# Performance work log

Measured on AMD Instinct MI355X. Metric: run time of the kernel, lower is better.

## Reference

```python
import jax, jax.numpy as jnp
import numpy as np

IMG = 224
WS = 8      # windows_size
STRIDE = 2
M = 1

def _dct_mat(size):
    i = np.arange(size)[:, None]
    j = np.arange(size)[None, :]
    scale = np.where(i == 0, np.sqrt(1.0 / size), np.sqrt(2.0 / size))
    return (scale * np.cos((j + 0.5) * np.pi * i / size)).astype(np.float32)

def _gen_filter(start, end, size):
    i = np.arange(size)[:, None]
    j = np.arange(size)[None, :]
    s = i + j
    return np.where((s > end) | (s < start), 0.0, 1.0).astype(np.float32)

def setup_inputs() -> dict:
    key = jax.random.key(0)
    x = jax.random.normal(key, (16, 3, IMG, IMG), dtype=jnp.float32)
    D = jnp.asarray(_dct_mat(WS))                       # [ws, ws] DCT matrix
    filt = jnp.asarray(_gen_filter(WS // 3, WS * 2, WS))  # high-pass base filter
    return {"x": x, "D": D, "filt": filt}

def reference(x, D, filt):
    b, c, H, W = x.shape
    n = (H - WS) // STRIDE + 1                 # patches per side (109)
    rows = jnp.arange(n)[:, None] * STRIDE + jnp.arange(WS)[None, :]  # [n, ws]
    # unfold: overlapping stride-2 patches -> [b, n, n, c, ws, ws]
    p = x[:, :, rows, :]                       # [b, c, n, ws, W]
    p = p[..., rows]                           # [b, c, n, ws, n, ws]
    p = p.transpose(0, 2, 4, 1, 3, 5)          # [b, n, n, c, ws, ws]
    # block DCT: D @ p @ D^T
    xd = jnp.einsum('pi,bmncij,qj->bmncpq', D, p, D)
    # filter (use_learnable=False, norm=False -> plain elementwise mask)
    y = xd * filt
    # block IDCT: D^T @ y @ D
    y = jnp.einsum('pi,bmncpq,qj->bmncij', D, y, D)
    # fold: overlap-add scatter back to [b, c, H, W]
    hh = rows[:, None, :, None]                # [n,1,ws,1]
    ww = rows[None, :, None, :]                # [1,n,1,ws]
    flat = hh * W + ww                         # [n,n,ws,ws] flat spatial index
    y_t = y.transpose(0, 3, 1, 2, 4, 5)        # [b, c, n, n, ws, ws]
    out = jnp.zeros((b, c, H * W), x.dtype).at[:, :, flat].add(y_t)
    return out.reshape(b, c, H, W)             # m=1 -> cat is identity
```

## Files before the change

kernel.cpp:

```cpp
#include <hip/hip_runtime.h>

#define IMG 224
#define NP 109
#define BC 48
#define NPIX (IMG * IMG)
#define TILE 56
#define QT 28
#define PT 31
#define XR 68
#define XC2 34


#define LOAD_D_SCALARS(D)                                                  \
    const float d0_0 = (D)[0], d0_1 = (D)[1], d0_2 = (D)[2], d0_3 = (D)[3],\
                d0_4 = (D)[4], d0_5 = (D)[5], d0_6 = (D)[6], d0_7 = (D)[7];\
    const float d1_0 = (D)[8],  d1_1 = (D)[9],  d1_2 = (D)[10],            \
                d1_3 = (D)[11], d1_4 = (D)[12], d1_5 = (D)[13],            \
                d1_6 = (D)[14], d1_7 = (D)[15];

__global__ __launch_bounds__(256) void fused_dct_kernel(
    const float* __restrict__ x, const float* __restrict__ D,
    const float* __restrict__ filt, float* __restrict__ out)
{
    __shared__ float x_s[XR * XR];
    __shared__ float ca_s[PT * PT];
    __shared__ float cb_s[PT * PT];
    __shared__ float cc_s[PT * PT];

    const int tid = threadIdx.x;
    const int h0 = blockIdx.y * TILE;
    const int w0 = blockIdx.x * TILE;
    const int bc = blockIdx.z;

    LOAD_D_SCALARS(D)
    const float w00 = 1.0f - filt[0];
    const float w01 = 1.0f - filt[1];
    const float w10 = 1.0f - filt[8];

    const float* xb = x + (size_t)bc * NPIX;

    for (int i = tid; i < XR * XC2; i += 256) {
        int r  = i / XC2;
        int c2 = i - r * XC2;
        int gr = h0 - 6 + r;
        int gc = w0 - 6 + 2 * c2;
        float2 v = make_float2(0.f, 0.f);
        if ((unsigned)gr < (unsigned)IMG && (unsigned)gc < (unsigned)IMG)
            v = *(const float2*)(xb + (size_t)gr * IMG + gc);
        *(float2*)&x_s[r * XR + 2 * c2] = v;
    }
    __syncthreads();

    const int pr0 = (h0 >> 1) - 3;
    const int pc0 = (w0 >> 1) - 3;
    for (int p = tid; p < PT * PT; p += 256) {
        int prl = p / PT;
        int pcl = p - prl * PT;
        const float* wnd = &x_s[(2 * prl) * XR + 2 * pcl];
        float c00 = 0.f, c01 = 0.f, c10 = 0.f;

#define C_ROW(i)                                                               \
        {                                                                      \
            const float2* prow = (const float2*)(wnd + (i) * XR);              \
            float2 v0 = prow[0], v1 = prow[1], v2 = prow[2], v3 = prow[3];     \
            float s = fmaf(v0.x, d0_0, fmaf(v0.y, d0_1,                        \
                      fmaf(v1.x, d0_2, fmaf(v1.y, d0_3,                        \
                      fmaf(v2.x, d0_4, fmaf(v2.y, d0_5,                        \
                      fmaf(v3.x, d0_6, v3.y * d0_7)))))));                     \
            float t = fmaf(v0.x, d1_0, fmaf(v0.y, d1_1,                        \
                      fmaf(v1.x, d1_2, fmaf(v1.y, d1_3,                        \
                      fmaf(v2.x, d1_4, fmaf(v2.y, d1_5,                        \
                      fmaf(v3.x, d1_6, v3.y * d1_7)))))));                     \
            c00 = fmaf(d0_##i, s, c00);                                        \
            c01 = fmaf(d0_##i, t, c01);                                        \
            c10 = fmaf(d1_##i, s, c10);                                        \
        }

        C_ROW(0) C_ROW(1) C_ROW(2) C_ROW(3)
        C_ROW(4) C_ROW(5) C_ROW(6) C_ROW(7)
#undef C_ROW

        bool valid = ((unsigned)(pr0 + prl) < (unsigned)NP) &&
                     ((unsigned)(pc0 + pcl) < (unsigned)NP);
        float m = valid ? 1.0f : 0.0f;
        ca_s[p] = c00 * w00 * m;
        cb_s[p] = c01 * w01 * m;
        cc_s[p] = c10 * w10 * m;
    }
    __syncthreads();

    const int qh0 = h0 >> 1, qw0 = w0 >> 1;
    float* ob = out + (size_t)bc * NPIX;
    for (int q = tid; q < QT * QT; q += 256) {
        int qhl = q / QT;
        int qwl = q - qhl * QT;

        float aee = 0.f, aeo = 0.f, aoe = 0.f, aoo = 0.f;

#define G_COL(kc, je, jo)                                                      \
        {                                                                      \
            int o = ro + (kc);                                                 \
            float a = ca_s[o], b = cb_s[o], c = cc_s[o];                       \
            Se = fmaf(a, d0_##je, fmaf(b, d1_##je, Se));                       \
            So = fmaf(a, d0_##jo, fmaf(b, d1_##jo, So));                       \
            Te = fmaf(c, d0_##je, Te);                                         \
            To = fmaf(c, d0_##jo, To);                                         \
        }

#define G_ROW(kr, ie, io)                                                      \
        {                                                                      \
            int ro = (qhl + (kr)) * PT + qwl;                                  \
            float Se = 0.f, So = 0.f, Te = 0.f, To = 0.f;                      \
            G_COL(0, 6, 7) G_COL(1, 4, 5) G_COL(2, 2, 3) G_COL(3, 0, 1)        \
            aee = fmaf(d0_##ie, Se, fmaf(d1_##ie, Te, aee));                   \
            aeo = fmaf(d0_##ie, So, fmaf(d1_##ie, To, aeo));                   \
            aoe = fmaf(d0_##io, Se, fmaf(d1_##io, Te, aoe));                   \
            aoo = fmaf(d0_##io, So, fmaf(d1_##io, To, aoo));                   \
        }

        G_ROW(0, 6, 7) G_ROW(1, 4, 5) G_ROW(2, 2, 3) G_ROW(3, 0, 1)
#undef G_ROW
#undef G_COL

        int qh = qh0 + qhl, qw = qw0 + qwl;
        int nvr = min(qh, NP - 1) - max(qh - 3, 0) + 1;
        int nvc = min(qw, NP - 1) - max(qw - 3, 0) + 1;
        float cnt = (float)(nvr * nvc);

        int lr = 2 * qhl + 6, lc = 2 * qwl + 6;
        float2 x0 = *(const float2*)&x_s[lr * XR + lc];
        float2 x1 = *(const float2*)&x_s[(lr + 1) * XR + lc];

        float2 o0, o1;
        o0.x = fmaf(cnt, x0.x, -aee);
        o0.y = fmaf(cnt, x0.y, -aeo);
        o1.x = fmaf(cnt, x1.x, -aoe);
        o1.y = fmaf(cnt, x1.y, -aoo);

        float* orp = ob + (size_t)(h0 + 2 * qhl) * IMG + (w0 + 2 * qwl);
        *(float2*)orp         = o0;
        *(float2*)(orp + IMG) = o1;
    }
}

extern "C" void kernel_launch(void* const* d_in, const int* in_sizes, int n_in,
                              void* d_out, int out_size, void* d_ws, size_t ws_size,
                              hipStream_t stream)
{
    const float* x    = (const float*)d_in[0];
    const float* D    = (const float*)d_in[1];
    const float* filt = (const float*)d_in[2];
    float* out        = (float*)d_out;

    dim3 grid(IMG / TILE, IMG / TILE, BC);
    fused_dct_kernel<<<grid, 256, 0, stream>>>(x, D, filt, out);
    (void)d_ws; (void)ws_size;
}
```

Measured before the change: 77.51 us.

## Split 2D separable passes into staged row/column passes through LDS

Makes the separable forward and inverse transforms two passes each: row sums over the input tile are computed once per row and stored in LDS, then reused by the column pass, instead of being recomputed for every overlapping patch. The input tile is also split into even and odd column planes for conflict-free scalar access. This removes redundant FMAs and shared-memory reads from overlapping windows, at the cost of extra LDS footprint, two more barriers, and extra LDS write/read traffic that may reduce occupancy.

Result: faster. 73.86 us (-4.7%).

```diff
diff --git a/kernel.cpp b/kernel.cpp
--- a/kernel.cpp
+++ b/kernel.cpp
@@ -18,14 +18,35 @@
                 d1_3 = (D)[11], d1_4 = (D)[12], d1_5 = (D)[13],            \
                 d1_6 = (D)[14], d1_7 = (D)[15];
 
+#define O_XE   0
+#define O_XO   (O_XE + XR * XC2)
+#define O_RS   (O_XO + XR * XC2)
+#define O_RT   (O_RS + XR * PT)
+#define O_RSE  O_RS
+#define O_RSO  (O_RSE + PT * QT)
+#define O_RTE  (O_RSO + PT * QT)
+#define O_RTO  (O_RTE + PT * QT)
+#define O_CA   (O_RT + XR * PT)
+#define O_CB   (O_CA + PT * PT)
+#define O_CC   (O_CB + PT * PT)
+#define LDS_FLOATS (O_CC + PT * PT)
+
 __global__ __launch_bounds__(256) void fused_dct_kernel(
     const float* __restrict__ x, const float* __restrict__ D,
     const float* __restrict__ filt, float* __restrict__ out)
 {
-    __shared__ float x_s[XR * XR];
-    __shared__ float ca_s[PT * PT];
-    __shared__ float cb_s[PT * PT];
-    __shared__ float cc_s[PT * PT];
+    __shared__ float lds[LDS_FLOATS];
+    float* const xe_s = lds + O_XE;
+    float* const xo_s = lds + O_XO;
+    float* const rs_s = lds + O_RS;
+    float* const rt_s = lds + O_RT;
+    float* const ca_s = lds + O_CA;
+    float* const cb_s = lds + O_CB;
+    float* const cc_s = lds + O_CC;
+    float* const RSe  = lds + O_RSE;
+    float* const RSo  = lds + O_RSO;
+    float* const RTe  = lds + O_RTE;
+    float* const RTo  = lds + O_RTO;
 
     const int tid = threadIdx.x;
     const int h0 = blockIdx.y * TILE;
@@ -47,7 +68,29 @@
         float2 v = make_float2(0.f, 0.f);
         if ((unsigned)gr < (unsigned)IMG && (unsigned)gc < (unsigned)IMG)
             v = *(const float2*)(xb + (size_t)gr * IMG + gc);
-        *(float2*)&x_s[r * XR + 2 * c2] = v;
+        xe_s[r * XC2 + c2] = v.x;
+        xo_s[r * XC2 + c2] = v.y;
+    }
+    __syncthreads();
+
+    for (int i = tid; i < XR * PT; i += 256) {
+        int r  = i / PT;
+        int pc = i - r * PT;
+        int b  = r * XC2 + pc;
+        float e0 = xe_s[b],     o0 = xo_s[b];
+        float e1 = xe_s[b + 1], o1 = xo_s[b + 1];
+        float e2 = xe_s[b + 2], o2 = xo_s[b + 2];
+        float e3 = xe_s[b + 3], o3 = xo_s[b + 3];
+        float s = fmaf(e0, d0_0, fmaf(o0, d0_1,
+                  fmaf(e1, d0_2, fmaf(o1, d0_3,
+                  fmaf(e2, d0_4, fmaf(o2, d0_5,
+                  fmaf(e3, d0_6, o3 * d0_7)))))));
+        float t = fmaf(e0, d1_0, fmaf(o0, d1_1,
+                  fmaf(e1, d1_2, fmaf(o1, d1_3,
+                  fmaf(e2, d1_4, fmaf(o2, d1_5,
+                  fmaf(e3, d1_6, o3 * d1_7)))))));
+        rs_s[i] = s;
+        rt_s[i] = t;
     }
     __syncthreads();
 
@@ -56,30 +99,19 @@
     for (int p = tid; p < PT * PT; p += 256) {
         int prl = p / PT;
         int pcl = p - prl * PT;
-        const float* wnd = &x_s[(2 * prl) * XR + 2 * pcl];
+        int b   = (2 * prl) * PT + pcl;
         float c00 = 0.f, c01 = 0.f, c10 = 0.f;
-
-#define C_ROW(i)                                                               \
+#define P3_ROW(i)                                                              \
         {                                                                      \
-            const float2* prow = (const float2*)(wnd + (i) * XR);              \
-            float2 v0 = prow[0], v1 = prow[1], v2 = prow[2], v3 = prow[3];     \
-            float s = fmaf(v0.x, d0_0, fmaf(v0.y, d0_1,                        \
-                      fmaf(v1.x, d0_2, fmaf(v1.y, d0_3,                        \
-                      fmaf(v2.x, d0_4, fmaf(v2.y, d0_5,                        \
-                      fmaf(v3.x, d0_6, v3.y * d0_7)))))));                     \
-            float t = fmaf(v0.x, d1_0, fmaf(v0.y, d1_1,                        \
-                      fmaf(v1.x, d1_2, fmaf(v1.y, d1_3,                        \
-                      fmaf(v2.x, d1_4, fmaf(v2.y, d1_5,                        \
-                      fmaf(v3.x, d1_6, v3.y * d1_7)))))));                     \
+            float s = rs_s[b + (i) * PT];                                      \
+            float t = rt_s[b + (i) * PT];                                      \
             c00 = fmaf(d0_##i, s, c00);                                        \
             c01 = fmaf(d0_##i, t, c01);                                        \
             c10 = fmaf(d1_##i, s, c10);                                        \
         }
-
-        C_ROW(0) C_ROW(1) C_ROW(2) C_ROW(3)
-        C_ROW(4) C_ROW(5) C_ROW(6) C_ROW(7)
-#undef C_ROW
-
+        P3_ROW(0) P3_ROW(1) P3_ROW(2) P3_ROW(3)
+        P3_ROW(4) P3_ROW(5) P3_ROW(6) P3_ROW(7)
+#undef P3_ROW
         bool valid = ((unsigned)(pr0 + prl) < (unsigned)NP) &&
                      ((unsigned)(pc0 + pcl) < (unsigned)NP);
         float m = valid ? 1.0f : 0.0f;
@@ -89,53 +121,60 @@
     }
     __syncthreads();
 
+    for (int i = tid; i < PT * QT; i += 256) {
+        int pr = i / QT;
+        int qw = i - pr * QT;
+        int b  = pr * PT + qw;
+        float se = 0.f, so = 0.f, te = 0.f, to = 0.f;
+#define P4_COL(kc, je, jo)                                                     \
+        {                                                                      \
+            float a = ca_s[b + (kc)];                                          \
+            float bb = cb_s[b + (kc)];                                         \
+            float c = cc_s[b + (kc)];                                          \
+            se = fmaf(a, d0_##je, fmaf(bb, d1_##je, se));                      \
+            so = fmaf(a, d0_##jo, fmaf(bb, d1_##jo, so));                      \
+            te = fmaf(c, d0_##je, te);                                         \
+            to = fmaf(c, d0_##jo, to);                                         \
+        }
+        P4_COL(0, 6, 7) P4_COL(1, 4, 5) P4_COL(2, 2, 3) P4_COL(3, 0, 1)
+#undef P4_COL
+        RSe[i] = se; RSo[i] = so; RTe[i] = te; RTo[i] = to;
+    }
+    __syncthreads();
+
     const int qh0 = h0 >> 1, qw0 = w0 >> 1;
     float* ob = out + (size_t)bc * NPIX;
     for (int q = tid; q < QT * QT; q += 256) {
         int qhl = q / QT;
         int qwl = q - qhl * QT;
-
+        int b   = qhl * QT + qwl;
         float aee = 0.f, aeo = 0.f, aoe = 0.f, aoo = 0.f;
-
-#define G_COL(kc, je, jo)                                                      \
+#define P5_ROW(kr, ie, io)                                                     \
         {                                                                      \
-            int o = ro + (kc);                                                 \
-            float a = ca_s[o], b = cb_s[o], c = cc_s[o];                       \
-            Se = fmaf(a, d0_##je, fmaf(b, d1_##je, Se));                       \
-            So = fmaf(a, d0_##jo, fmaf(b, d1_##jo, So));                       \
-            Te = fmaf(c, d0_##je, Te);                                         \
-            To = fmaf(c, d0_##jo, To);                                         \
+            int o = b + (kr) * QT;                                             \
+            float se = RSe[o], so = RSo[o], te = RTe[o], to = RTo[o];          \
+            aee = fmaf(d0_##ie, se, fmaf(d1_##ie, te, aee));                   \
+            aeo = fmaf(d0_##ie, so, fmaf(d1_##ie, to, aeo));                   \
+            aoe = fmaf(d0_##io, se, fmaf(d1_##io, te, aoe));                   \
+            aoo = fmaf(d0_##io, so, fmaf(d1_##io, to, aoo));                   \
         }
-
-#define G_ROW(kr, ie, io)                                                      \
-        {                                                                      \
-            int ro = (qhl + (kr)) * PT + qwl;                                  \
-            float Se = 0.f, So = 0.f, Te = 0.f, To = 0.f;                      \
-            G_COL(0, 6, 7) G_COL(1, 4, 5) G_COL(2, 2, 3) G_COL(3, 0, 1)        \
-            aee = fmaf(d0_##ie, Se, fmaf(d1_##ie, Te, aee));                   \
-            aeo = fmaf(d0_##ie, So, fmaf(d1_##ie, To, aeo));                   \
-            aoe = fmaf(d0_##io, Se, fmaf(d1_##io, Te, aoe));                   \
-            aoo = fmaf(d0_##io, So, fmaf(d1_##io, To, aoo));                   \
-        }
-
-        G_ROW(0, 6, 7) G_ROW(1, 4, 5) G_ROW(2, 2, 3) G_ROW(3, 0, 1)
-#undef G_ROW
-#undef G_COL
+        P5_ROW(0, 6, 7) P5_ROW(1, 4, 5) P5_ROW(2, 2, 3) P5_ROW(3, 0, 1)
+#undef P5_ROW
 
         int qh = qh0 + qhl, qw = qw0 + qwl;
         int nvr = min(qh, NP - 1) - max(qh - 3, 0) + 1;
         int nvc = min(qw, NP - 1) - max(qw - 3, 0) + 1;
         float cnt = (float)(nvr * nvc);
 
-        int lr = 2 * qhl + 6, lc = 2 * qwl + 6;
-        float2 x0 = *(const float2*)&x_s[lr * XR + lc];
-        float2 x1 = *(const float2*)&x_s[(lr + 1) * XR + lc];
+        int xr = (2 * qhl + 6) * XC2 + (qwl + 3);
+        float x00 = xe_s[xr],       x01 = xo_s[xr];
+        float x10 = xe_s[xr + XC2], x11 = xo_s[xr + XC2];
 
         float2 o0, o1;
-        o0.x = fmaf(cnt, x0.x, -aee);
-        o0.y = fmaf(cnt, x0.y, -aeo);
-        o1.x = fmaf(cnt, x1.x, -aoe);
-        o1.y = fmaf(cnt, x1.y, -aoo);
+        o0.x = fmaf(cnt, x00, -aee);
+        o0.y = fmaf(cnt, x01, -aeo);
+        o1.x = fmaf(cnt, x10, -aoe);
+        o1.y = fmaf(cnt, x11, -aoo);
 
         float* orp = ob + (size_t)(h0 + 2 * qhl) * IMG + (w0 + 2 * qwl);
         *(float2*)orp         = o0;
```
